# Kernel optimization log

Hardware: AMD Instinct MI355X
Metric: run time of the kernel (lower is better)

Reference implementation:

```python
import jax, jax.numpy as jnp
import numpy as np
import math

B, S, D, P = 128, 512, 1024, 32
TEMP, BETA = 0.1, 0.4

def _lin_init(k, din, dout):
    k1, k2 = jax.random.split(k)
    s = 1.0 / math.sqrt(din)
    W = jax.random.uniform(k1, (din, dout), minval=-s, maxval=s, dtype=jnp.float32)
    b = jax.random.uniform(k2, (dout,), minval=-s, maxval=s, dtype=jnp.float32)
    return W, b

def setup_inputs():
    key = jax.random.key(0)
    ks = jax.random.split(key, 20)
    inp = {
        'x_head': jax.random.normal(ks[0], (B, D), dtype=jnp.float32),
        'x_rel': jax.random.normal(ks[1], (B, S, D), dtype=jnp.float32),
        'x_tail': jax.random.normal(ks[2], (B, S, D), dtype=jnp.float32),
        'x_mask': (jax.random.uniform(ks[3], (B, S)) < 0.9).astype(jnp.float32),
        'x_img': jax.random.normal(ks[4], (B, D), dtype=jnp.float32),
    }
    names = [('wf1', 2 * D, D), ('wf2', D, D), ('wk', D, D), ('wv', D, D),
             ('wp', D, D), ('wiq', D, D), ('whq', D, D), ('wlt', D, D),
             ('wli', D, D), ('wltr', D, D), ('wgt', D, D), ('wgi', D, D)]
    for i, (nm, din, dout) in enumerate(names):
        W, b = _lin_init(ks[5 + i], din, dout)
        inp[nm] = W
        inp['b' + nm[1:]] = b
    return inp

def reference(x_head, x_rel, x_tail, x_mask, x_img,
              wf1, bf1, wf2, bf2, wk, bk, wv, bv, wp, bp,
              wiq, biq, whq, bhq, wlt, blt, wli, bli,
              wltr, bltr, wgt, bgt, wgi, bgi):
    # reltail feature combine: MLP(cat[tail, rel]) residual onto tail (eval: no dropout)
    feat = jnp.concatenate([x_tail, x_rel], axis=-1)            # [B,S,2D]
    h = jax.nn.leaky_relu(feat @ wf1 + bf1, negative_slope=0.01)
    x_reltail = x_tail + (h @ wf2 + bf2)                        # [B,S,D]
    keys = x_reltail @ wk + bk                                  # [B,S,D]
    values = x_reltail @ wv + bv                                # [B,S,D]
    iq = x_img @ wiq + biq                                      # [B,D]
    hq = x_head @ whq + bhq                                     # [B,D]
    inv_sqrt_d = 1.0 / math.sqrt(D)
    s1 = jnp.einsum('bd,bsd->bs', iq, keys) * inv_sqrt_d        # [B,S]
    s2 = jnp.einsum('bd,bsd->bs', hq, keys) * inv_sqrt_d
    neg_inf = jnp.finfo(s1.dtype).min
    valid = x_mask > 0.01
    s1 = jnp.where(valid, s1, neg_inf)
    s2 = jnp.where(valid, s2, neg_inf)
    scores = (s1 * BETA + s2 * (1.0 - BETA)) / TEMP
    attn = jax.nn.softmax(scores, axis=-1)                      # [B,S]
    # top-p sparsify: keep only the P largest weights (no renormalization)
    _, top_idx = jax.lax.top_k(attn, P)                         # [B,P]
    top_mask = jnp.zeros_like(attn).at[jnp.arange(B)[:, None], top_idx].set(1.0)
    attn = attn * top_mask
    ctx = jnp.einsum('bs,bsd->bd', attn, values)                # [B,D]
    x_triple = ctx @ wp + bp
    # gated projection combine
    text_out = x_head @ wlt + blt
    img_out = x_img @ wli + bli
    triple_out = x_triple @ wltr + bltr
    text_gate = jax.nn.sigmoid(x_head @ wgt + bgt)
    img_gate = jax.nn.sigmoid(x_img @ wgi + bgi)
    return triple_out + text_out * text_gate + img_out * img_gate
```

## Files before the change

kernel.cpp:

```cpp
#include <hip/hip_runtime.h>
#include <math.h>


typedef short bf16x8 __attribute__((ext_vector_type(8)));
typedef float f32x4 __attribute__((ext_vector_type(4)));

typedef const __attribute__((address_space(1))) void* gp_t;
typedef __attribute__((address_space(3))) void* lp_t;

__device__ __forceinline__ void ld16(const void* g, void* l) {
  __builtin_amdgcn_global_load_lds((gp_t)g, (lp_t)l, 16, 0, 0);
}

__device__ __forceinline__ unsigned int f2b(float f) {
  unsigned int u = __builtin_bit_cast(unsigned int, f);
  u = (u + 0x7FFFu + ((u >> 16) & 1u)) >> 16;
  return u & 0xFFFFu;
}
__device__ __forceinline__ float b2f(unsigned short s) {
  unsigned int u = ((unsigned int)s) << 16;
  return __builtin_bit_cast(float, u);
}
__device__ __forceinline__ float b2f_lo(unsigned int u) { return __builtin_bit_cast(float, u << 16); }
__device__ __forceinline__ float b2f_hi(unsigned int u) { return __builtin_bit_cast(float, u & 0xFFFF0000u); }
__device__ __forceinline__ unsigned int pack2(float lo, float hi) { return f2b(lo) | (f2b(hi) << 16); }

__global__ void cvt_feat_k(const float4* __restrict__ tail, const float4* __restrict__ rel,
                           uint4* __restrict__ feat, const float* __restrict__ qk,
                           float* __restrict__ sc) {
  unsigned t = threadIdx.x;
  unsigned i = blockIdx.x * 256 + t;
  unsigned row = blockIdx.x, c = t;
  bool isrel = c >= 128u;
  const float4* src = isrel ? rel : tail;
  unsigned s = row * 256u + (c & 127u) * 2u;
  float4 a = src[s], b = src[s + 1];
  uint4 o;
  o.x = pack2(a.x, a.y); o.y = pack2(a.z, a.w);
  o.z = pack2(b.x, b.y); o.w = pack2(b.z, b.w);
  feat[i] = o;
  float part = 0.f;
  if (!isrel) {
    const float* qr = qk + (size_t)(row >> 9) * 1024 + c * 8;
    part = a.x * qr[0] + a.y * qr[1] + a.z * qr[2] + a.w * qr[3]
         + b.x * qr[4] + b.y * qr[5] + b.z * qr[6] + b.w * qr[7];
  }
  for (int off = 32; off > 0; off >>= 1) part += __shfl_down(part, off);
  if ((t & 63u) == 0u && !isrel) atomicAdd(sc + row, part);
}

__global__ void transpose_cvt_k(const float* __restrict__ W, unsigned short* __restrict__ Wt,
                                int K, int N) {
  __shared__ float tile[32][33];
  int t = threadIdx.x;
  int tx = t & 31, ty = t >> 5;
  int n0 = blockIdx.x * 32, k0 = blockIdx.y * 32;
  #pragma unroll
  for (int i = 0; i < 32; i += 8)
    tile[ty + i][tx] = W[(size_t)(k0 + ty + i) * N + n0 + tx];
  __syncthreads();
  #pragma unroll
  for (int i = 0; i < 32; i += 8)
    Wt[(size_t)(n0 + ty + i) * K + k0 + tx] = (unsigned short)f2b(tile[tx][ty + i]);
}

struct SJob { const float* A; const float* W; const float* u; const float* rs;
              const float* A2; float* C; int transB; int pad; };
struct SJobs { SJob j[6]; };

__global__ __launch_bounds__(256) void sgemm_k(SJobs jobs, int K) {
  SJob jb = jobs.j[blockIdx.z];
  __shared__ float At[32 * 132];
  __shared__ float Wt_[32 * 36];
  int t = threadIdx.x;
  int n0 = blockIdx.x * 32;
  int kchunk = K / gridDim.y;
  int kbase = blockIdx.y * kchunk;
  int tn = t & 7, tm = t >> 3;
  float acc[4][4] = {};
  for (int kt = 0; kt < kchunk; kt += 32) {
    int k0 = kbase + kt;
    #pragma unroll
    for (int i = 0; i < 16; ++i) {
      int f = i * 256 + t;
      int r = f >> 5, c = f & 31;
      float v = jb.A[(size_t)r * K + k0 + c];
      if (jb.A2) v += jb.A2[(size_t)r * K + k0 + c];
      if (jb.u) v += (jb.rs ? jb.rs[r] : 1.0f) * jb.u[k0 + c];
      At[c * 132 + r] = v;
    }
    #pragma unroll
    for (int i = 0; i < 4; ++i) {
      int f = i * 256 + t;
      if (!jb.transB) { int k = f >> 5, n = f & 31; Wt_[k * 36 + n] = jb.W[(size_t)(k0 + k) * 1024 + n0 + n]; }
      else            { int n = f >> 5, k = f & 31; Wt_[k * 36 + n] = jb.W[(size_t)(n0 + n) * K + k0 + k]; }
    }
    __syncthreads();
    #pragma unroll
    for (int kk = 0; kk < 32; ++kk) {
      float4 av = *(const float4*)&At[kk * 132 + tm * 4];
      float4 wv4 = *(const float4*)&Wt_[kk * 36 + tn * 4];
      float ar[4] = {av.x, av.y, av.z, av.w};
      float wr[4] = {wv4.x, wv4.y, wv4.z, wv4.w};
      #pragma unroll
      for (int r = 0; r < 4; ++r)
        #pragma unroll
        for (int c = 0; c < 4; ++c) acc[r][c] += ar[r] * wr[c];
    }
    __syncthreads();
  }
  #pragma unroll
  for (int r = 0; r < 4; ++r)
    #pragma unroll
    for (int c = 0; c < 4; ++c)
      atomicAdd(jb.C + (size_t)(tm * 4 + r) * 1024 + n0 + tn * 4 + c, acc[r][c]);
}

__global__ void ew1_k(const float* __restrict__ riq, const float* __restrict__ rhq,
                      const float* __restrict__ rt, const float* __restrict__ ri,
                      const float* __restrict__ rtg, const float* __restrict__ rig,
                      const float* __restrict__ biq, const float* __restrict__ bhq,
                      const float* __restrict__ blt, const float* __restrict__ bli,
                      const float* __restrict__ bgt, const float* __restrict__ bgi,
                      float* __restrict__ qc, float* __restrict__ pout) {
  int idx = blockIdx.x * 256 + threadIdx.x;
  int n = idx & 1023;
  float iq = riq[idx] + biq[n];
  float hq = rhq[idx] + bhq[n];
  qc[idx] = 0.3125f * (0.4f * iq + 0.6f * hq);
  float tg = 1.0f / (1.0f + expf(-(rtg[idx] + bgt[n])));
  float ig = 1.0f / (1.0f + expf(-(rig[idx] + bgi[n])));
  pout[idx] = (rt[idx] + blt[n]) * tg + (ri[idx] + bli[n]) * ig;
}

__global__ void cvec_k(const float* __restrict__ qc, const float* __restrict__ bk,
                       const float* __restrict__ qk, const float* __restrict__ bf2,
                       float* __restrict__ cv) {
  int b = blockIdx.x, l = threadIdx.x;
  const float4* a = (const float4*)(qc + (size_t)b * 1024);
  const float4* k4 = (const float4*)bk;
  const float4* a2 = (const float4*)(qk + (size_t)b * 1024);
  const float4* k42 = (const float4*)bf2;
  float acc = 0.f;
  #pragma unroll
  for (int i = 0; i < 4; ++i) {
    float4 x = a[l + i * 64], y = k4[l + i * 64];
    acc += x.x * y.x + x.y * y.y + x.z * y.z + x.w * y.w;
    float4 x2 = a2[l + i * 64], y2 = k42[l + i * 64];
    acc += x2.x * y2.x + x2.y * y2.y + x2.z * y2.z + x2.w * y2.w;
  }
  for (int off = 32; off > 0; off >>= 1) acc += __shfl_down(acc, off);
  if (l == 0) cv[b] = acc;
}

__global__ __launch_bounds__(512, 2) void gemm256_k(
    const unsigned short* __restrict__ A, const unsigned short* __restrict__ Wt,
    const float* __restrict__ bias, const float* __restrict__ wq2,
    unsigned short* __restrict__ C, float* __restrict__ sc, int M, int N, int K) {
  extern __shared__ __align__(16) unsigned short Sm[];
  int t = threadIdx.x;
  int l = t & 63, w = t >> 6;

  int L = blockIdx.x;
  int xcd = L & 7, j = L >> 3;
  int n_t = j & 3;
  int m_t = (j >> 2) * 8 + xcd;
  int m0 = m_t * 256, n0 = n_t * 256;
  int wm = (w >> 2) * 128, wn = (w & 3) * 64;

  int r0 = t >> 2, slot = t & 3;
  int col8 = slot ^ ((r0 >> 1) & 3);
  const unsigned short* Ag = A + (size_t)(m0 + r0) * K + col8 * 8;
  const unsigned short* Bg = Wt + (size_t)(n0 + r0) * K + col8 * 8;
  size_t rowadv = (size_t)128 * K;
  unsigned short* dA0 = Sm + t * 8;
  unsigned short* dA1 = Sm + 4096 + t * 8;
  unsigned short* dB0 = Sm + 8192 + t * 8;
  unsigned short* dB1 = Sm + 12288 + t * 8;

  int lm = l & 15, q = l >> 4;
  int aoff[8], boff[4];
  #pragma unroll
  for (int i = 0; i < 8; ++i) {
    int ra = wm + i * 16 + lm;
    aoff[i] = ra * 32 + ((q ^ ((ra >> 1) & 3)) * 8);
  }
  #pragma unroll
  for (int i = 0; i < 4; ++i) {
    int rb = wn + i * 16 + lm;
    boff[i] = rb * 32 + ((q ^ ((rb >> 1) & 3)) * 8);
  }

  f32x4 acc[8][4];
  #pragma unroll
  for (int i = 0; i < 8; ++i)
    #pragma unroll
    for (int jj = 0; jj < 4; ++jj) acc[i][jj] = (f32x4){0.f, 0.f, 0.f, 0.f};

  int NT = K >> 5;

#define STAGE(buf, kt) do {                                     \
    const unsigned short* a_ = Ag + (size_t)(kt) * 32;          \
    const unsigned short* b_ = Bg + (size_t)(kt) * 32;          \
    ld16(a_,          (buf) * 16384 + dA0);                     \
    ld16(a_ + rowadv, (buf) * 16384 + dA1);                     \
    ld16(b_,          (buf) * 16384 + dB0);                     \
    ld16(b_ + rowadv, (buf) * 16384 + dB1);                     \
  } while (0)

#define COMPUTE(cur) do {                                       \
    const unsigned short* base = Sm + (cur) * 16384;            \
    bf16x8 af[8], bfv[4];                                       \
    _Pragma("unroll")                                           \
    for (int i = 0; i < 8; ++i) af[i] = *(const bf16x8*)(base + aoff[i]);        \
    _Pragma("unroll")                                           \
    for (int i = 0; i < 4; ++i) bfv[i] = *(const bf16x8*)(base + 8192 + boff[i]);\
    __builtin_amdgcn_s_setprio(1);                              \
    _Pragma("unroll")                                           \
    for (int mi = 0; mi < 8; ++mi)                              \
      _Pragma("unroll")                                         \
      for (int ni = 0; ni < 4; ++ni)                            \
        acc[mi][ni] = __builtin_amdgcn_mfma_f32_16x16x32_bf16(af[mi], bfv[ni], acc[mi][ni], 0, 0, 0); \
    __builtin_amdgcn_s_setprio(0);                              \
  } while (0)

  STAGE(0, 0);
  STAGE(1, 1);
  STAGE(2, 2);
  for (int kt = 0; kt + 3 < NT; ++kt) {
    STAGE((kt + 3) & 3, kt + 3);
    asm volatile("s_waitcnt vmcnt(12)\n\ts_barrier" ::: "memory");
    COMPUTE(kt & 3);
    asm volatile("s_barrier" ::: "memory");
  }
  asm volatile("s_waitcnt vmcnt(8)\n\ts_barrier" ::: "memory");
  COMPUTE((NT - 3) & 3);
  asm volatile("s_barrier" ::: "memory");
  asm volatile("s_waitcnt vmcnt(4)\n\ts_barrier" ::: "memory");
  COMPUTE((NT - 2) & 3);
  asm volatile("s_barrier" ::: "memory");
  asm volatile("s_waitcnt vmcnt(0)\n\ts_barrier" ::: "memory");
  COMPUTE((NT - 1) & 3);
  asm volatile("s_barrier" ::: "memory");

  int lr = q * 4;
  #pragma unroll
  for (int h = 0; h < 2; ++h) {
    if ((w >> 2) == h) {
      #pragma unroll
      for (int mi = 0; mi < 8; ++mi) {
        #pragma unroll
        for (int ni = 0; ni < 4; ++ni) {
          int cn = wn + ni * 16 + lm;
          float bb = bias[n0 + cn];
          #pragma unroll
          for (int r = 0; r < 4; ++r) {
            int row = mi * 16 + lr + r;
            float v = acc[mi][ni][r] + bb;
            v = v > 0.f ? v : 0.01f * v;
            Sm[row * 256 + cn] = (unsigned short)f2b(v);
          }
        }
      }
    }
    __syncthreads();
    #pragma unroll
    for (int p = 0; p < 8; ++p) {
      int idx = p * 512 + t;
      int rr = idx >> 5;
      int c8 = (idx & 31) * 8;
      uint4 cs = *(const uint4*)(Sm + rr * 256 + c8);
      *(uint4*)(C + (size_t)(m0 + h * 128 + rr) * N + n0 + c8) = cs;
    }
    {
      int row = t >> 2, quarter = t & 3;
      int b = (m0 + h * 128) >> 9;
      const uint4* cr = (const uint4*)(Sm + row * 256 + quarter * 64);
      const float4* wr = (const float4*)(wq2 + (size_t)b * 1024 + n0 + quarter * 64);
      float part = 0.f;
      #pragma unroll
      for (int jj = 0; jj < 8; ++jj) {
        uint4 cw = cr[jj];
        float4 w0 = wr[jj * 2], w1 = wr[jj * 2 + 1];
        part += b2f_lo(cw.x) * w0.x + b2f_hi(cw.x) * w0.y;
        part += b2f_lo(cw.y) * w0.z + b2f_hi(cw.y) * w0.w;
        part += b2f_lo(cw.z) * w1.x + b2f_hi(cw.z) * w1.y;
        part += b2f_lo(cw.w) * w1.z + b2f_hi(cw.w) * w1.w;
      }
      part += __shfl_xor(part, 1);
      part += __shfl_xor(part, 2);
      if (quarter == 0) atomicAdd(sc + m0 + h * 128 + row, part);
    }
    __syncthreads();
  }
#undef STAGE
#undef COMPUTE
}

__global__ __launch_bounds__(256) void topk_ctx_k(const float* __restrict__ sc,
                                                  const float* __restrict__ mask,
                                                  const float* __restrict__ cv,
                                                  const float* __restrict__ xtail,
                                                  const unsigned short* __restrict__ h,
                                                  float* __restrict__ ctxtail, float* __restrict__ gh,
                                                  float* __restrict__ asum) {
  int b = blockIdx.x, t = threadIdx.x;
  __shared__ float sv[512];
  __shared__ float red[256];
  __shared__ float topw[32];
  __shared__ int topi[32];
  float cvb = cv[b];
  float r0 = sc[b * 512 + t], r1 = sc[b * 512 + 256 + t];
  float v0 = (mask[b * 512 + t] > 0.01f) ? (r0 + cvb) : -__builtin_inff();
  float v1 = (mask[b * 512 + 256 + t] > 0.01f) ? (r1 + cvb) : -__builtin_inff();
  sv[t] = v0; sv[t + 256] = v1;
  red[t] = fmaxf(v0, v1);
  __syncthreads();
  for (int s = 128; s > 0; s >>= 1) { if (t < s) red[t] = fmaxf(red[t], red[t + s]); __syncthreads(); }
  float mx = red[0];
  __syncthreads();
  float e0 = expf(v0 - mx), e1 = expf(v1 - mx);
  red[t] = e0 + e1;
  __syncthreads();
  for (int s = 128; s > 0; s >>= 1) { if (t < s) red[t] += red[t + s]; __syncthreads(); }
  float inv = 1.0f / red[0];
  __syncthreads();
  sv[t] = e0 * inv; sv[t + 256] = e1 * inv;
  __syncthreads();
  if (t < 64) {
    float v[8];
    int base = t * 8;
    #pragma unroll
    for (int jj = 0; jj < 8; ++jj) v[jj] = sv[base + jj];
    for (int it = 0; it < 32; ++it) {
      float bv = v[0]; int bj = 0;
      #pragma unroll
      for (int jj = 1; jj < 8; ++jj) if (v[jj] > bv) { bv = v[jj]; bj = jj; }
      int bidx = base + bj;
      #pragma unroll
      for (int off = 32; off > 0; off >>= 1) {
        float ov = __shfl_xor(bv, off);
        int oi = __shfl_xor(bidx, off);
        if (ov > bv || (ov == bv && oi < bidx)) { bv = ov; bidx = oi; }
      }
      if (t == (bidx >> 3)) v[bidx & 7] = -1.0f;
      if (t == 0) { topw[it] = bv; topi[it] = bidx; }
    }
  }
  __syncthreads();
  #pragma unroll
  for (int dd = 0; dd < 4; ++dd) {
    int d = t + dd * 256;
    float at = 0.f, ah = 0.f;
    for (int jj = 0; jj < 32; ++jj) {
      size_t ro = (size_t)(b * 512 + topi[jj]) * 1024 + d;
      at += topw[jj] * xtail[ro];
      ah += topw[jj] * b2f(h[ro]);
    }
    ctxtail[(size_t)b * 1024 + d] = at;
    gh[(size_t)b * 1024 + d] = ah;
  }
  if (t == 0) {
    float s = 0.f;
    for (int jj = 0; jj < 32; ++jj) s += topw[jj];
    asum[b] = s;
  }
}

__global__ void ew2_k(const float* __restrict__ r3, const float* __restrict__ bltr,
                      const float* __restrict__ pout, float* __restrict__ out) {
  int idx = blockIdx.x * 256 + threadIdx.x;
  out[idx] = r3[idx] + bltr[idx & 1023] + pout[idx];
}

extern "C" void kernel_launch(void* const* d_in, const int* in_sizes, int n_in,
                              void* d_out, int out_size, void* d_ws, size_t ws_size,
                              hipStream_t stream) {
  const float* x_head = (const float*)d_in[0];
  const float* x_rel  = (const float*)d_in[1];
  const float* x_tail = (const float*)d_in[2];
  const float* x_mask = (const float*)d_in[3];
  const float* x_img  = (const float*)d_in[4];
  const float* wf1 = (const float*)d_in[5];  const float* bf1 = (const float*)d_in[6];
  const float* wf2 = (const float*)d_in[7];  const float* bf2 = (const float*)d_in[8];
  const float* wk  = (const float*)d_in[9];  const float* bk  = (const float*)d_in[10];
  const float* wv  = (const float*)d_in[11]; const float* bv  = (const float*)d_in[12];
  const float* wp  = (const float*)d_in[13]; const float* bp  = (const float*)d_in[14];
  const float* wiq = (const float*)d_in[15]; const float* biq = (const float*)d_in[16];
  const float* whq = (const float*)d_in[17]; const float* bhq = (const float*)d_in[18];
  const float* wlt = (const float*)d_in[19]; const float* blt = (const float*)d_in[20];
  const float* wli = (const float*)d_in[21]; const float* bli = (const float*)d_in[22];
  const float* wltr= (const float*)d_in[23]; const float* bltr= (const float*)d_in[24];
  const float* wgt = (const float*)d_in[25]; const float* bgt = (const float*)d_in[26];
  const float* wgi = (const float*)d_in[27]; const float* bgi = (const float*)d_in[28];
  float* out = (float*)d_out;
  char* ws = (char*)d_ws;

  unsigned short* feat = (unsigned short*)(ws);
  unsigned short* hbuf = (unsigned short*)(ws + 268435456ull);
  unsigned short* wf1t = (unsigned short*)(ws + 402653184ull);
  char* z = ws + 406847488ull;
  float* raw_iq = (float*)(z);
  float* raw_hq = (float*)(z + 524288);
  float* raw_t  = (float*)(z + 1048576);
  float* raw_i  = (float*)(z + 1572864);
  float* raw_tg = (float*)(z + 2097152);
  float* raw_ig = (float*)(z + 2621440);
  float* raw_q  = (float*)(z + 3145728);
  float* wq2    = (float*)(z + 3670016);
  float* rawG   = (float*)(z + 4194304);
  float* rawL1  = (float*)(z + 4718592);
  float* rawL2  = (float*)(z + 5242880);
  float* rawL3  = (float*)(z + 5767168);
  float* sc     = (float*)(z + 6291456);
  float* qc      = (float*)(ws + 413663232ull);
  float* pout    = (float*)(ws + 414187520ull);
  float* cv      = (float*)(ws + 414711808ull);
  float* ctxtail = (float*)(ws + 414715904ull);
  float* gh      = (float*)(ws + 415240192ull);
  float* asum    = (float*)(ws + 415764480ull);

  hipFuncSetAttribute((const void*)gemm256_k,
                      hipFuncAttributeMaxDynamicSharedMemorySize, 131072);

  hipMemsetAsync(z, 0, 6553600, stream);

  SJobs j6 = {};
  j6.j[0] = SJob{x_img,  wiq, nullptr, nullptr, nullptr, raw_iq, 0, 0};
  j6.j[1] = SJob{x_head, whq, nullptr, nullptr, nullptr, raw_hq, 0, 0};
  j6.j[2] = SJob{x_head, wlt, nullptr, nullptr, nullptr, raw_t,  0, 0};
  j6.j[3] = SJob{x_img,  wli, nullptr, nullptr, nullptr, raw_i,  0, 0};
  j6.j[4] = SJob{x_head, wgt, nullptr, nullptr, nullptr, raw_tg, 0, 0};
  j6.j[5] = SJob{x_img,  wgi, nullptr, nullptr, nullptr, raw_ig, 0, 0};
  sgemm_k<<<dim3(32, 4, 6), 256, 0, stream>>>(j6, 1024);

  ew1_k<<<512, 256, 0, stream>>>(raw_iq, raw_hq, raw_t, raw_i, raw_tg, raw_ig,
                                 biq, bhq, blt, bli, bgt, bgi, qc, pout);

  SJobs jq = {};
  jq.j[0] = SJob{qc, wk, nullptr, nullptr, nullptr, raw_q, 1, 0};
  sgemm_k<<<dim3(32, 8, 1), 256, 0, stream>>>(jq, 1024);
  jq.j[0] = SJob{raw_q, wf2, nullptr, nullptr, nullptr, wq2, 1, 0};
  sgemm_k<<<dim3(32, 8, 1), 256, 0, stream>>>(jq, 1024);
  cvec_k<<<128, 64, 0, stream>>>(qc, bk, raw_q, bf2, cv);

  cvt_feat_k<<<65536, 256, 0, stream>>>((const float4*)x_tail, (const float4*)x_rel,
                                        (uint4*)feat, raw_q, sc);
  transpose_cvt_k<<<dim3(32, 64), 256, 0, stream>>>(wf1, wf1t, 2048, 1024);

  gemm256_k<<<1024, 512, 131072, stream>>>(feat, wf1t, bf1, wq2, hbuf, sc, 65536, 1024, 2048);

  topk_ctx_k<<<128, 256, 0, stream>>>(sc, x_mask, cv, x_tail, hbuf, ctxtail, gh, asum);

  SJobs jl = {};
  jl.j[0] = SJob{gh, wf2, nullptr, nullptr, nullptr, rawG, 0, 0};
  sgemm_k<<<dim3(32, 8, 1), 256, 0, stream>>>(jl, 1024);
  jl.j[0] = SJob{rawG, wv, bf2, asum, ctxtail, rawL1, 0, 0};
  sgemm_k<<<dim3(32, 8, 1), 256, 0, stream>>>(jl, 1024);
  jl.j[0] = SJob{rawL1, wp, bv, asum, nullptr, rawL2, 0, 0};
  sgemm_k<<<dim3(32, 8, 1), 256, 0, stream>>>(jl, 1024);
  jl.j[0] = SJob{rawL2, wltr, bp, nullptr, nullptr, rawL3, 0, 0};
  sgemm_k<<<dim3(32, 8, 1), 256, 0, stream>>>(jl, 1024);
  ew2_k<<<512, 256, 0, stream>>>(rawL3, bltr, pout, out);
}
```

Measured before the change: 1.362 ms.

## Restructure GEMM main loop into double-buffered 64-wide K tiles with interleaved loads

```diff
diff --git a/kernel.cpp b/kernel.cpp
--- a/kernel.cpp
+++ b/kernel.cpp
@@ -168,28 +168,21 @@
   int m0 = m_t * 256, n0 = n_t * 256;
   int wm = (w >> 2) * 128, wn = (w & 3) * 64;
 
-  int r0 = t >> 2, slot = t & 3;
-  int col8 = slot ^ ((r0 >> 1) & 3);
-  const unsigned short* Ag = A + (size_t)(m0 + r0) * K + col8 * 8;
-  const unsigned short* Bg = Wt + (size_t)(n0 + r0) * K + col8 * 8;
-  size_t rowadv = (size_t)128 * K;
-  unsigned short* dA0 = Sm + t * 8;
-  unsigned short* dA1 = Sm + 4096 + t * 8;
-  unsigned short* dB0 = Sm + 8192 + t * 8;
-  unsigned short* dB1 = Sm + 12288 + t * 8;
+  int rw = t >> 2;
+  int csw = (t & 3) ^ ((rw >> 1) & 3);
+  const unsigned short* A0g = A + (size_t)(m0 + rw) * K + csw * 8;
+  const unsigned short* A1g = A + (size_t)(m0 + 128 + rw) * K + csw * 8;
+  const unsigned short* B0g = Wt + (size_t)(n0 + rw) * K + csw * 8;
+  const unsigned short* B1g = Wt + (size_t)(n0 + 128 + rw) * K + csw * 8;
+  unsigned short* dst = Sm + t * 8;
 
   int lm = l & 15, q = l >> 4;
+  int slotx = (q ^ ((lm >> 1) & 3)) * 8;
   int aoff[8], boff[4];
   #pragma unroll
-  for (int i = 0; i < 8; ++i) {
-    int ra = wm + i * 16 + lm;
-    aoff[i] = ra * 32 + ((q ^ ((ra >> 1) & 3)) * 8);
-  }
-  #pragma unroll
-  for (int i = 0; i < 4; ++i) {
-    int rb = wn + i * 16 + lm;
-    boff[i] = rb * 32 + ((q ^ ((rb >> 1) & 3)) * 8);
-  }
+  for (int i = 0; i < 8; ++i) aoff[i] = (wm + i * 16 + lm) * 32 + slotx;
+  #pragma unroll
+  for (int i = 0; i < 4; ++i) boff[i] = 8192 + (wn + i * 16 + lm) * 32 + slotx;
 
   f32x4 acc[8][4];
   #pragma unroll
@@ -197,51 +190,76 @@
     #pragma unroll
     for (int jj = 0; jj < 4; ++jj) acc[i][jj] = (f32x4){0.f, 0.f, 0.f, 0.f};
 
-  int NT = K >> 5;
-
-#define STAGE(buf, kt) do {                                     \
-    const unsigned short* a_ = Ag + (size_t)(kt) * 32;          \
-    const unsigned short* b_ = Bg + (size_t)(kt) * 32;          \
-    ld16(a_,          (buf) * 16384 + dA0);                     \
-    ld16(a_ + rowadv, (buf) * 16384 + dA1);                     \
-    ld16(b_,          (buf) * 16384 + dB0);                     \
-    ld16(b_ + rowadv, (buf) * 16384 + dB1);                     \
-  } while (0)
-
-#define COMPUTE(cur) do {                                       \
-    const unsigned short* base = Sm + (cur) * 16384;            \
-    bf16x8 af[8], bfv[4];                                       \
-    _Pragma("unroll")                                           \
-    for (int i = 0; i < 8; ++i) af[i] = *(const bf16x8*)(base + aoff[i]);        \
-    _Pragma("unroll")                                           \
-    for (int i = 0; i < 4; ++i) bfv[i] = *(const bf16x8*)(base + 8192 + boff[i]);\
-    __builtin_amdgcn_s_setprio(1);                              \
-    _Pragma("unroll")                                           \
-    for (int mi = 0; mi < 8; ++mi)                              \
-      _Pragma("unroll")                                         \
-      for (int ni = 0; ni < 4; ++ni)                            \
-        acc[mi][ni] = __builtin_amdgcn_mfma_f32_16x16x32_bf16(af[mi], bfv[ni], acc[mi][ni], 0, 0, 0); \
-    __builtin_amdgcn_s_setprio(0);                              \
-  } while (0)
-
-  STAGE(0, 0);
-  STAGE(1, 1);
-  STAGE(2, 2);
-  for (int kt = 0; kt + 3 < NT; ++kt) {
-    STAGE((kt + 3) & 3, kt + 3);
-    asm volatile("s_waitcnt vmcnt(12)\n\ts_barrier" ::: "memory");
-    COMPUTE(kt & 3);
-    asm volatile("s_barrier" ::: "memory");
-  }
-  asm volatile("s_waitcnt vmcnt(8)\n\ts_barrier" ::: "memory");
-  COMPUTE((NT - 3) & 3);
-  asm volatile("s_barrier" ::: "memory");
+  int NT = K >> 6;
+
+#define MFMA16(mbase, ks)                                                 \
+    __builtin_amdgcn_s_setprio(1);                                        \
+    _Pragma("unroll")                                                     \
+    for (int mi = 0; mi < 4; ++mi)                                        \
+      _Pragma("unroll")                                                   \
+      for (int ni = 0; ni < 4; ++ni)                                      \
+        acc[(mbase) + mi][ni] =                                           \
+          __builtin_amdgcn_mfma_f32_16x16x32_bf16(aF[mi], bF[ni], acc[(mbase) + mi][ni], 0, 0, 0); \
+    __builtin_amdgcn_s_setprio(0);
+
+  ld16(A0g, dst);          ld16(A1g, dst + 4096);
+  ld16(B0g, dst + 8192);   ld16(B1g, dst + 12288);
+  ld16(A0g + 32, dst + 16384); ld16(A1g + 32, dst + 20480);
+  ld16(B0g + 32, dst + 24576); ld16(B1g + 32, dst + 28672);
   asm volatile("s_waitcnt vmcnt(4)\n\ts_barrier" ::: "memory");
-  COMPUTE((NT - 2) & 3);
-  asm volatile("s_barrier" ::: "memory");
+
+  for (int kt = 0; kt < NT; ++kt) {
+    const unsigned short* base = Sm + (kt & 1) * 32768;
+    unsigned short* nd = dst + ((kt & 1) ^ 1) * 32768;
+    size_t ksrc = (size_t)((kt + 1 < NT) ? (kt + 1) : kt) * 64;
+    bf16x8 aF[4], bF[4];
+
+    #pragma unroll
+    for (int i = 0; i < 4; ++i) bF[i] = *(const bf16x8*)(base + boff[i]);
+    #pragma unroll
+    for (int i = 0; i < 4; ++i) aF[i] = *(const bf16x8*)(base + aoff[i]);
+    ld16(A0g + ksrc, nd);
+    ld16(A1g + ksrc, nd + 4096);
+    __builtin_amdgcn_s_barrier();
+    asm volatile("s_waitcnt lgkmcnt(0)" ::: "memory");
+    __builtin_amdgcn_sched_barrier(0);
+    MFMA16(0, 0)
+    __builtin_amdgcn_s_barrier();
+
+    #pragma unroll
+    for (int i = 0; i < 4; ++i) aF[i] = *(const bf16x8*)(base + aoff[4 + i]);
+    ld16(B0g + ksrc, nd + 8192);
+    ld16(B1g + ksrc, nd + 12288);
+    __builtin_amdgcn_s_barrier();
+    asm volatile("s_waitcnt lgkmcnt(0)" ::: "memory");
+    __builtin_amdgcn_sched_barrier(0);
+    MFMA16(4, 0)
+    asm volatile("s_waitcnt vmcnt(4)\n\ts_barrier" ::: "memory");
+
+    #pragma unroll
+    for (int i = 0; i < 4; ++i) bF[i] = *(const bf16x8*)(base + 16384 + boff[i]);
+    #pragma unroll
+    for (int i = 0; i < 4; ++i) aF[i] = *(const bf16x8*)(base + 16384 + aoff[i]);
+    ld16(A0g + ksrc + 32, nd + 16384);
+    ld16(A1g + ksrc + 32, nd + 20480);
+    __builtin_amdgcn_s_barrier();
+    asm volatile("s_waitcnt lgkmcnt(0)" ::: "memory");
+    __builtin_amdgcn_sched_barrier(0);
+    MFMA16(0, 1)
+    __builtin_amdgcn_s_barrier();
+
+    #pragma unroll
+    for (int i = 0; i < 4; ++i) aF[i] = *(const bf16x8*)(base + 16384 + aoff[4 + i]);
+    ld16(B0g + ksrc + 32, nd + 24576);
+    ld16(B1g + ksrc + 32, nd + 28672);
+    __builtin_amdgcn_s_barrier();
+    asm volatile("s_waitcnt lgkmcnt(0)" ::: "memory");
+    __builtin_amdgcn_sched_barrier(0);
+    MFMA16(4, 1)
+    asm volatile("s_waitcnt vmcnt(4)\n\ts_barrier" ::: "memory");
+  }
   asm volatile("s_waitcnt vmcnt(0)\n\ts_barrier" ::: "memory");
-  COMPUTE((NT - 1) & 3);
-  asm volatile("s_barrier" ::: "memory");
+#undef MFMA16
 
   int lr = q * 4;
   #pragma unroll
@@ -293,8 +311,6 @@
     }
     __syncthreads();
   }
-#undef STAGE
-#undef COMPUTE
 }
 
 __global__ __launch_bounds__(256) void topk_ctx_k(const float* __restrict__ sc,
```

New measurement: 1.349 ms. No clear change (-1.0%).
